# Kernel tuning notes

Hardware: AMD Instinct MI355X
Metric: run time of the kernel (lower is better)

Reference implementation:

```python
import jax, jax.numpy as jnp
import numpy as np

B, D, O = 131072, 128, 256

def setup_inputs() -> dict:
    key = jax.random.key(0)
    k1, k2, k3 = jax.random.split(key, 3)
    x = jax.random.normal(k1, (B, D), dtype=jnp.float32)
    weight = jax.random.normal(k2, (O, D), dtype=jnp.float32)
    bias = jax.random.normal(k3, (O,), dtype=jnp.float32)
    return {"x": x, "weight": weight, "bias": bias}

def reference(x, weight, bias):
    # Original: (x[:,None,:] * W[None,:,:]).sum(-1) == linear contraction over D.
    z = jnp.einsum('bd,od->bo', x, weight) + bias  # [B, O]
    # hyperoperation_order == 2 -> elementwise square; activation is None.
    return z * z
```

## Files before the change

kernel.cpp:

```cpp
#include <hip/hip_runtime.h>
#include <hip/hip_bf16.h>


#define B_ROWS 131072
#define D_DIM  128
#define O_DIM  256
#define THREADS 256
#define NBLOCKS 2048
#define TILES 4
#define ROWS_PER_BLOCK (TILES * 16)
#define LDS_PITCH 68

using bf16x8 = __attribute__((ext_vector_type(8))) short;
using f32x4  = __attribute__((ext_vector_type(4))) float;

__device__ __forceinline__ short bf16rne(float f) {
    unsigned u = __builtin_bit_cast(unsigned, f);
    u += 0x7FFFu + ((u >> 16) & 1u);
    return (short)(u >> 16);
}

__device__ __forceinline__ bf16x8 pack8(float4 h0, float4 h1) {
    bf16x8 t;
    t[0] = bf16rne(h0.x); t[1] = bf16rne(h0.y);
    t[2] = bf16rne(h0.z); t[3] = bf16rne(h0.w);
    t[4] = bf16rne(h1.x); t[5] = bf16rne(h1.y);
    t[6] = bf16rne(h1.z); t[7] = bf16rne(h1.w);
    return t;
}

__global__ __launch_bounds__(THREADS, 3)
void hyper_linear_sq_kernel(const float* __restrict__ x,
                            const float* __restrict__ weight,
                            const float* __restrict__ bias,
                            float* __restrict__ out) {
    __shared__ float lds[4][16][LDS_PITCH];

    const int lane  = threadIdx.x & 63;
    const int wid   = threadIdx.x >> 6;
    const int n16   = lane & 15;
    const int quad  = lane >> 4;
    const int cbase = wid * 64;

    bf16x8 bfrag[4][4];
    #pragma unroll
    for (int ct = 0; ct < 4; ++ct) {
        const float* wr = weight + (cbase + ct * 16 + n16) * D_DIM + quad * 8;
        #pragma unroll
        for (int ks = 0; ks < 4; ++ks) {
            float4 h0 = *(const float4*)(wr + ks * 32);
            float4 h1 = *(const float4*)(wr + ks * 32 + 4);
            bfrag[ct][ks] = pack8(h0, h1);
        }
    }

    float bv[4];
    #pragma unroll
    for (int ct = 0; ct < 4; ++ct) bv[ct] = bias[cbase + ct * 16 + n16];

    const int rowbase0 = blockIdx.x * ROWS_PER_BLOCK;
    const float* xbase = x + ((long)rowbase0 + n16) * D_DIM + quad * 8;

    float4 raw[8];
    #pragma unroll
    for (int ks = 0; ks < 4; ++ks) {
        raw[2 * ks]     = *(const float4*)(xbase + ks * 32);
        raw[2 * ks + 1] = *(const float4*)(xbase + ks * 32 + 4);
    }

    #pragma unroll
    for (int t = 0; t < TILES; ++t) {
        bf16x8 a[4];
        #pragma unroll
        for (int ks = 0; ks < 4; ++ks) a[ks] = pack8(raw[2 * ks], raw[2 * ks + 1]);

        float4 rawn[8];
        if (t + 1 < TILES) {
            const float* xn = xbase + (long)(t + 1) * 16 * D_DIM;
            #pragma unroll
            for (int ks = 0; ks < 4; ++ks) {
                rawn[2 * ks]     = *(const float4*)(xn + ks * 32);
                rawn[2 * ks + 1] = *(const float4*)(xn + ks * 32 + 4);
            }
        }

        f32x4 acc[4];
        #pragma unroll
        for (int ct = 0; ct < 4; ++ct) acc[ct] = (f32x4){0.f, 0.f, 0.f, 0.f};

        #pragma unroll
        for (int ks = 0; ks < 4; ++ks) {
            #pragma unroll
            for (int ct = 0; ct < 4; ++ct) {
                acc[ct] = __builtin_amdgcn_mfma_f32_16x16x32_bf16(a[ks], bfrag[ct][ks], acc[ct], 0, 0, 0);
            }
        }

        #pragma unroll
        for (int ct = 0; ct < 4; ++ct) {
            #pragma unroll
            for (int r = 0; r < 4; ++r) {
                float z = acc[ct][r] + bv[ct];
                lds[wid][quad * 4 + r][ct * 16 + n16] = z * z;
            }
        }
        #pragma unroll
        for (int s = 0; s < 4; ++s) {
            f32x4 v = *(const f32x4*)&lds[wid][s * 4 + quad][n16 * 4];
            long row = rowbase0 + t * 16 + s * 4 + quad;
            __builtin_nontemporal_store(v, (f32x4*)(out + row * O_DIM + cbase + n16 * 4));
        }

        if (t + 1 < TILES) {
            #pragma unroll
            for (int i = 0; i < 8; ++i) raw[i] = rawn[i];
        }
    }
}

extern "C" void kernel_launch(void* const* d_in, const int* in_sizes, int n_in,
                              void* d_out, int out_size, void* d_ws, size_t ws_size,
                              hipStream_t stream) {
    const float* x    = (const float*)d_in[0];
    const float* w    = (const float*)d_in[1];
    const float* bias = (const float*)d_in[2];
    float* out        = (float*)d_out;
    hipLaunchKernelGGL(hyper_linear_sq_kernel, dim3(NBLOCKS), dim3(THREADS), 0, stream,
                       x, w, bias, out);
}
```

Before: 225.4 us.

## Stage x tiles through LDS as bf16 with coalesced row loads

Each half-wave now reads one full contiguous row of x, instead of lanes fetching scattered 32-byte chunks across 16 rows. The data is converted to bf16 and written into a per-wave, double-buffered LDS tile. MFMA A-fragments are then read back from LDS, and the current buffer is reused as float scratch for the output transpose. This targets poor global-load coalescing on the input stream, at the cost of doubling LDS use and adding an extra LDS write/read round-trip per tile.

```diff
diff --git a/kernel.cpp b/kernel.cpp
--- a/kernel.cpp
+++ b/kernel.cpp
@@ -9,7 +9,7 @@
 #define NBLOCKS 2048
 #define TILES 4
 #define ROWS_PER_BLOCK (TILES * 16)
-#define LDS_PITCH 68
+#define XT_PITCH 136
 
 using bf16x8 = __attribute__((ext_vector_type(8))) short;
 using f32x4  = __attribute__((ext_vector_type(4))) float;
@@ -18,6 +18,13 @@
     unsigned u = __builtin_bit_cast(unsigned, f);
     u += 0x7FFFu + ((u >> 16) & 1u);
     return (short)(u >> 16);
+}
+
+__device__ __forceinline__ short4 pack4(float4 v) {
+    short4 p;
+    p.x = bf16rne(v.x); p.y = bf16rne(v.y);
+    p.z = bf16rne(v.z); p.w = bf16rne(v.w);
+    return p;
 }
 
 __device__ __forceinline__ bf16x8 pack8(float4 h0, float4 h1) {
@@ -34,13 +41,15 @@
                             const float* __restrict__ weight,
                             const float* __restrict__ bias,
                             float* __restrict__ out) {
-    __shared__ float lds[4][16][LDS_PITCH];
+    __shared__ short xt[2][4][16 * XT_PITCH];
 
     const int lane  = threadIdx.x & 63;
     const int wid   = threadIdx.x >> 6;
     const int n16   = lane & 15;
     const int quad  = lane >> 4;
     const int cbase = wid * 64;
+    const int half  = lane >> 5;
+    const int l32   = lane & 31;
 
     bf16x8 bfrag[4][4];
     #pragma unroll
@@ -58,31 +67,35 @@
     #pragma unroll
     for (int ct = 0; ct < 4; ++ct) bv[ct] = bias[cbase + ct * 16 + n16];
 
-    const int rowbase0 = blockIdx.x * ROWS_PER_BLOCK;
-    const float* xbase = x + ((long)rowbase0 + n16) * D_DIM + quad * 8;
+    const long rowbase0 = (long)blockIdx.x * ROWS_PER_BLOCK;
+    const float* xld = x + (rowbase0 + half) * D_DIM + l32 * 4;
 
-    float4 raw[8];
-    #pragma unroll
-    for (int ks = 0; ks < 4; ++ks) {
-        raw[2 * ks]     = *(const float4*)(xbase + ks * 32);
-        raw[2 * ks + 1] = *(const float4*)(xbase + ks * 32 + 4);
+    {
+        float4 r0[8];
+        #pragma unroll
+        for (int i = 0; i < 8; ++i)
+            r0[i] = *(const float4*)(xld + (long)(2 * i) * D_DIM);
+        #pragma unroll
+        for (int i = 0; i < 8; ++i)
+            *(short4*)&xt[0][wid][(2 * i + half) * XT_PITCH + l32 * 4] = pack4(r0[i]);
     }
 
     #pragma unroll
     for (int t = 0; t < TILES; ++t) {
+        const int buf = t & 1;
+
+        float4 rn[8];
+        if (t + 1 < TILES) {
+            const float* xn = xld + (long)(t + 1) * 16 * D_DIM;
+            #pragma unroll
+            for (int i = 0; i < 8; ++i)
+                rn[i] = *(const float4*)(xn + (long)(2 * i) * D_DIM);
+        }
+
         bf16x8 a[4];
         #pragma unroll
-        for (int ks = 0; ks < 4; ++ks) a[ks] = pack8(raw[2 * ks], raw[2 * ks + 1]);
-
-        float4 rawn[8];
-        if (t + 1 < TILES) {
-            const float* xn = xbase + (long)(t + 1) * 16 * D_DIM;
-            #pragma unroll
-            for (int ks = 0; ks < 4; ++ks) {
-                rawn[2 * ks]     = *(const float4*)(xn + ks * 32);
-                rawn[2 * ks + 1] = *(const float4*)(xn + ks * 32 + 4);
-            }
-        }
+        for (int ks = 0; ks < 4; ++ks)
+            a[ks] = *(const bf16x8*)&xt[buf][wid][n16 * XT_PITCH + ks * 32 + quad * 8];
 
         f32x4 acc[4];
         #pragma unroll
@@ -96,24 +109,26 @@
             }
         }
 
+        if (t + 1 < TILES) {
+            #pragma unroll
+            for (int i = 0; i < 8; ++i)
+                *(short4*)&xt[buf ^ 1][wid][(2 * i + half) * XT_PITCH + l32 * 4] = pack4(rn[i]);
+        }
+
+        float* ft = (float*)&xt[buf][wid][0];
         #pragma unroll
         for (int ct = 0; ct < 4; ++ct) {
             #pragma unroll
             for (int r = 0; r < 4; ++r) {
                 float z = acc[ct][r] + bv[ct];
-                lds[wid][quad * 4 + r][ct * 16 + n16] = z * z;
+                ft[(quad * 4 + r) * 68 + ct * 16 + n16] = z * z;
             }
         }
         #pragma unroll
         for (int s = 0; s < 4; ++s) {
-            f32x4 v = *(const f32x4*)&lds[wid][s * 4 + quad][n16 * 4];
+            f32x4 v = *(const f32x4*)&ft[(s * 4 + quad) * 68 + n16 * 4];
             long row = rowbase0 + t * 16 + s * 4 + quad;
             __builtin_nontemporal_store(v, (f32x4*)(out + row * O_DIM + cbase + n16 * 4));
-        }
-
-        if (t + 1 < TILES) {
-            #pragma unroll
-            for (int i = 0; i < 8; ++i) raw[i] = rawn[i];
         }
     }
 }
```

Result: slower. 262.2 us (+16.3%).
